# Kernel optimization log

Measured on AMD Instinct MI355X. Metric: run time of the kernel, lower is better.

Reference implementation:

```python
import jax, jax.numpy as jnp
import numpy as np

EMBED_DIM = 128
N_HEADS = 8
TANH_CLIP = 10.0
NEG_INF = -1e9


def setup_inputs() -> dict:
    key = jax.random.key(0)
    k1, k2, k3, k4 = jax.random.split(key, 4)
    B, N, D = 512, 200, EMBED_DIM
    s = 1.0 / np.sqrt(D)
    return {
        "embeddings": jax.random.normal(k1, (B, N, D), dtype=jnp.float32),
        "W_node": jax.random.uniform(k2, (D, 3 * D), jnp.float32, -s, s),
        "W_fixed": jax.random.uniform(k3, (D, D), jnp.float32, -s, s),
        "W_step": jax.random.uniform(k4, (D, D), jnp.float32, -s, s),
    }


def _decode(embeddings, W_node, W_fixed, W_step):
    B, N, D = embeddings.shape
    H = N_HEADS
    dk = D // H

    # Precompute (once): glimpse K/V and logit K, plus fixed graph context.
    proj = embeddings @ W_node                      # [B,N,3D]
    gK, gV, lK = jnp.split(proj, 3, axis=-1)
    gK = gK.reshape(B, N, H, dk).transpose(0, 2, 1, 3)   # [B,H,N,dk]
    gV = gV.reshape(B, N, H, dk).transpose(0, 2, 1, 3)   # [B,H,N,dk]
    graph_emb = embeddings.mean(axis=1)             # [B,D]
    fixed_ctx = graph_emb @ W_fixed                 # [B,D]

    inv_sqrt_dk = 1.0 / jnp.sqrt(jnp.asarray(dk, embeddings.dtype))
    inv_sqrt_d = 1.0 / jnp.sqrt(jnp.asarray(D, embeddings.dtype))
    batch_idx = jnp.arange(B)

    def step(carry, _):
        visited, ctx_emb = carry                    # [B,N] bool, [B,D]
        q = fixed_ctx + ctx_emb @ W_step            # [B,D]
        qh = q.reshape(B, H, dk)                    # [B,H,dk]
        # glimpse multi-head attention (mask_inner=True)
        compat = jnp.einsum('bhd,bhnd->bhn', qh, gK) * inv_sqrt_dk
        compat = jnp.where(visited[:, None, :], NEG_INF, compat)
        attn = jax.nn.softmax(compat, axis=-1)
        glimpse = jnp.einsum('bhn,bhnd->bhd', attn, gV).reshape(B, D)
        # single-head logits with tanh clipping (mask_logits=True)
        logits = jnp.einsum('bd,bnd->bn', glimpse, lK) * inv_sqrt_d
        logits = TANH_CLIP * jnp.tanh(logits)
        logits = jnp.where(visited, NEG_INF, logits)
        log_p = jax.nn.log_softmax(logits, axis=-1)  # [B,N]
        sel = jnp.argmax(log_p, axis=-1)             # greedy [B]
        visited = visited.at[batch_idx, sel].set(True)
        ctx_emb = embeddings[batch_idx, sel]         # next step context
        return (visited, ctx_emb), (log_p, sel)

    init = (jnp.zeros((B, N), dtype=bool), graph_emb)
    _, (log_ps, sels) = jax.lax.scan(step, init, None, length=N)
    return log_ps.transpose(1, 0, 2), sels.transpose(1, 0)  # [B,T,N], [B,T]


def reference(embeddings, W_node, W_fixed, W_step):
    log_p, pi = _decode(embeddings, W_node, W_fixed, W_step)
    return log_p, pi
```

## Files before the change

### kernel.cpp

```cpp
#include <hip/hip_runtime.h>
#include <math.h>


#define Bsz 512
#define Nn  200
#define Dd  128
#define TANH_CLIP 10.0f
#define NEG_INF  -1e9f
#define LOG2E 1.4426950408889634f
#define LN2   0.6931471805599453f

__device__ __forceinline__ float dot4(float4 a, float4 b) {
    return a.x*b.x + a.y*b.y + a.z*b.z + a.w*b.w;
}
__device__ __forceinline__ float rdlane(float v, int l) {
    union { float f; int i; } u; u.f = v;
    u.i = __builtin_amdgcn_readlane(u.i, l);
    return u.f;
}

__global__ __launch_bounds__(256, 3) void proj_kernel(
    const float* __restrict__ emb, const float* __restrict__ Wn,
    float* __restrict__ gk, float* __restrict__ gv, float* __restrict__ lk)
{
    const int bid = blockIdx.x;
    const int cg  = bid % 3;
    const int rowBase = (bid / 3) * 64;
    const int t  = threadIdx.x;
    const int c4 = t & 31;
    const int r8 = t >> 5;

    __shared__ __align__(16) float wn_s[64][128];
    __shared__ __align__(16) float e_s[64][68];

    float acc[8][4];
#pragma unroll
    for (int j = 0; j < 8; ++j)
#pragma unroll
        for (int m = 0; m < 4; ++m) acc[j][m] = 0.f;

    for (int kh = 0; kh < 2; ++kh) {
#pragma unroll
        for (int i = 0; i < 8; ++i) {
            const int idx = t + 256 * i;
            const int kr = idx >> 5, cc = (idx & 31) * 4;
            *(float4*)&wn_s[kr][cc] =
                *(const float4*)&Wn[(size_t)(kh * 64 + kr) * 384 + 128 * cg + cc];
        }
#pragma unroll
        for (int i = 0; i < 4; ++i) {
            const int idx = t + 256 * i;
            const int rr = idx >> 4, kk4 = (idx & 15) * 4;
            *(float4*)&e_s[rr][kk4] =
                *(const float4*)&emb[(size_t)(rowBase + rr) * Dd + kh * 64 + kk4];
        }
        __syncthreads();

#pragma unroll
        for (int k4 = 0; k4 < 16; ++k4) {
            float4 er[8];
#pragma unroll
            for (int j = 0; j < 8; ++j)
                er[j] = *(const float4*)&e_s[8 * r8 + j][4 * k4];
#pragma unroll
            for (int m = 0; m < 4; ++m) {
                const float4 wv = *(const float4*)&wn_s[4 * k4 + m][4 * c4];
#pragma unroll
                for (int j = 0; j < 8; ++j) {
                    const float ev = (m == 0) ? er[j].x : (m == 1) ? er[j].y
                                   : (m == 2) ? er[j].z : er[j].w;
                    acc[j][0] = fmaf(ev, wv.x, acc[j][0]);
                    acc[j][1] = fmaf(ev, wv.y, acc[j][1]);
                    acc[j][2] = fmaf(ev, wv.z, acc[j][2]);
                    acc[j][3] = fmaf(ev, wv.w, acc[j][3]);
                }
            }
        }
        __syncthreads();
    }

    float* out = (cg == 0) ? gk : (cg == 1) ? gv : lk;
#pragma unroll
    for (int j = 0; j < 8; ++j) {
        float4 v; v.x = acc[j][0]; v.y = acc[j][1]; v.z = acc[j][2]; v.w = acc[j][3];
        *(float4*)&out[(size_t)(rowBase + 8 * r8 + j) * Dd + 4 * c4] = v;
    }
}

__global__ __launch_bounds__(512, 1) void decode_kernel(
    const float* __restrict__ emb,
    const float* __restrict__ Wf,
    const float* __restrict__ Wsp,
    const float* __restrict__ gk, const float* __restrict__ gv,
    const float* __restrict__ lk,
    float* __restrict__ out_logp,
    float* __restrict__ out_pi)
{
    const int b    = blockIdx.x;
    const int t    = threadIdx.x;
    const int lane = t & 63;
    const int w    = t >> 6;
    const int g    = t >> 7;
    const int d    = t & 127;
    const int jq   = lane >> 2;
    const int cq   = lane & 3;

    __shared__ __align__(16) float qall_s[201 * Dd];
    __shared__ __align__(16) float wchunk_s[16][Dd];
    __shared__ __align__(16) float sm2[8][256];
    __shared__ __align__(16) float red[4][Dd];
    __shared__ __align__(16) float ctx0_s[Dd];
    __shared__ __align__(16) float fixedc_s[Dd];
    __shared__ __align__(16) float glim_s[Dd];
    __shared__ __align__(16) float logits_s[Nn];

    const float inv_sqrt_d = 0.08838834764831845f;
    const float QSCALE = 0.25f * LOG2E;

    const float* embB = emb + (size_t)b * Nn * Dd;
    const float* gkB  = gk  + (size_t)b * Nn * Dd;
    const float* gvB  = gv  + (size_t)b * Nn * Dd;
    const float* lkB  = lk  + (size_t)b * Nn * Dd;

    {
        const float4* e4  = (const float4*)embB;
        float4*       es4 = (float4*)qall_s;
#pragma unroll
        for (int it = 0; it < 12; ++it) es4[t + 512 * it] = e4[t + 512 * it];
        if (t < 256) es4[t + 6144] = e4[t + 6144];
    }
    __syncthreads();

    {
        float s = 0.f;
#pragma unroll
        for (int k = 0; k < 50; ++k) s += qall_s[(50 * g + k) * Dd + d];
        red[g][d] = s;
    }
    __syncthreads();
    if (t < 128) ctx0_s[t] = (red[0][t] + red[1][t] + red[2][t] + red[3][t]) * (1.0f / 200.0f);
    __syncthreads();

    {
        float s = 0.f;
#pragma unroll
        for (int j = 0; j < 32; ++j)
            s = fmaf(ctx0_s[32 * g + j], Wf[(32 * g + j) * Dd + d], s);
        red[g][d] = s;
    }
    __syncthreads();
    if (t < 128) {
        fixedc_s[t] = (red[0][t] + red[1][t] + red[2][t] + red[3][t]) * QSCALE;
        qall_s[200 * Dd + t] = ctx0_s[t];
    }
    __syncthreads();

    float qr[52];
#pragma unroll
    for (int i = 0; i < 52; ++i) qr[i] = 0.f;

    for (int kc = 0; kc < 8; ++kc) {
        {
            const int kr = t >> 5, cc = (t & 31) * 4;
            *(float4*)&wchunk_s[kr][cc] =
                *(const float4*)&Wsp[(size_t)(16 * kc + kr) * Dd + cc];
        }
        __syncthreads();
#pragma unroll
        for (int i = 0; i < 52; ++i) {
            const int r = 52 * g + i;
            if (r < 201) {
#pragma unroll
                for (int j4 = 0; j4 < 4; ++j4) {
                    const float4 ev = *(const float4*)&qall_s[r * Dd + 16 * kc + 4 * j4];
                    qr[i] = fmaf(ev.x, wchunk_s[4 * j4 + 0][d], qr[i]);
                    qr[i] = fmaf(ev.y, wchunk_s[4 * j4 + 1][d], qr[i]);
                    qr[i] = fmaf(ev.z, wchunk_s[4 * j4 + 2][d], qr[i]);
                    qr[i] = fmaf(ev.w, wchunk_s[4 * j4 + 3][d], qr[i]);
                }
            }
        }
        __syncthreads();
    }
#pragma unroll
    for (int i = 0; i < 52; ++i) {
        const int r = 52 * g + i;
        if (r < 201) qall_s[r * Dd + d] = qr[i] * QSCALE;
    }
    __syncthreads();

    float4 gk0[4], gk1[4], gk2[4], gk3[4];
    float  gv_r[52];
    float4 lk_r[16];
    {
        const float4* s0 = (const float4*)(gkB + (size_t)(lane      ) * Dd + 16 * w);
        const float4* s1 = (const float4*)(gkB + (size_t)(lane +  64) * Dd + 16 * w);
        const float4* s2 = (const float4*)(gkB + (size_t)(lane + 128) * Dd + 16 * w);
        const int n3 = (lane < 8) ? lane + 192 : 199;
        const float4* s3 = (const float4*)(gkB + (size_t)n3 * Dd + 16 * w);
#pragma unroll
        for (int i = 0; i < 4; ++i) { gk0[i]=s0[i]; gk1[i]=s1[i]; gk2[i]=s2[i]; gk3[i]=s3[i]; }
    }
#pragma unroll
    for (int k = 0; k < 52; ++k) {
        int r = 52 * cq + k; r = r < 200 ? r : 199;
        gv_r[k] = gvB[(size_t)r * Dd + 16 * w + jq];
    }
    if (t < 400) {
        const float4* src = (const float4*)(lkB + (size_t)(t >> 1) * Dd + (t & 1) * 64);
#pragma unroll
        for (int i = 0; i < 16; ++i) lk_r[i] = src[i];
    } else {
#pragma unroll
        for (int i = 0; i < 16; ++i) lk_r[i] = float4{0, 0, 0, 0};
    }
    const float fc_q = fixedc_s[16 * w + jq];

    unsigned long long vis0 = 0, vis1 = 0, vis2 = 0, vis3 = 0;
    int sel_prev = 200;

    for (int step = 0; step < Nn; ++step) {
        float s = qall_s[sel_prev * Dd + 16 * w + jq] + fc_q;
        const float q0  = rdlane(s, 0),  q1  = rdlane(s, 4),  q2  = rdlane(s, 8),  q3  = rdlane(s, 12);
        const float q4  = rdlane(s, 16), q5  = rdlane(s, 20), q6  = rdlane(s, 24), q7  = rdlane(s, 28);
        const float q8  = rdlane(s, 32), q9  = rdlane(s, 36), q10 = rdlane(s, 40), q11 = rdlane(s, 44);
        const float q12 = rdlane(s, 48), q13 = rdlane(s, 52), q14 = rdlane(s, 56), q15 = rdlane(s, 60);

#define DOT16(G) (fmaf((G)[0].x,q0, fmaf((G)[0].y,q1, fmaf((G)[0].z,q2, fmaf((G)[0].w,q3, \
                  fmaf((G)[1].x,q4, fmaf((G)[1].y,q5, fmaf((G)[1].z,q6, fmaf((G)[1].w,q7, \
                  fmaf((G)[2].x,q8, fmaf((G)[2].y,q9, fmaf((G)[2].z,q10,fmaf((G)[2].w,q11,\
                  fmaf((G)[3].x,q12,fmaf((G)[3].y,q13,fmaf((G)[3].z,q14,(G)[3].w*q15))))))))))))))))

        float x0 = DOT16(gk0), x1 = DOT16(gk1), x2 = DOT16(gk2), x3 = DOT16(gk3);
        x0 = ((vis0 >> lane) & 1ull) ? -1e30f : x0;
        x1 = ((vis1 >> lane) & 1ull) ? -1e30f : x1;
        x2 = ((vis2 >> lane) & 1ull) ? -1e30f : x2;
        x3 = (lane < 8 && !((vis3 >> lane) & 1ull)) ? x3 : -1e30f;
        const float p0 = exp2f(x0), p1 = exp2f(x1), p2 = exp2f(x2), p3 = exp2f(x3);
        {
            float* prow = &sm2[w][0];
            prow[lane      ] = p0;
            prow[lane +  64] = p1;
            prow[lane + 128] = p2;
            prow[lane + 192] = p3;
        }
        float ps = (p0 + p1) + (p2 + p3);
#pragma unroll
        for (int off = 1; off < 64; off <<= 1) ps += __shfl_xor(ps, off);
        const float invps = 1.0f / ps;

        {
            const float* a = &sm2[w][52 * cq];
            float s0 = 0.f, s1 = 0.f, s2 = 0.f, s3 = 0.f;
#pragma unroll
            for (int k4 = 0; k4 < 13; ++k4) {
                const float4 av = ((const float4*)a)[k4];
                s0 = fmaf(av.x, gv_r[4 * k4 + 0], s0);
                s1 = fmaf(av.y, gv_r[4 * k4 + 1], s1);
                s2 = fmaf(av.z, gv_r[4 * k4 + 2], s2);
                s3 = fmaf(av.w, gv_r[4 * k4 + 3], s3);
            }
            float gsum = (s0 + s1) + (s2 + s3);
            gsum += __shfl_xor(gsum, 1);
            gsum += __shfl_xor(gsum, 2);
            if (cq == 0) glim_s[16 * w + jq] = gsum * invps;
        }
        __syncthreads();

        if (t < 400) {
            const int n = t >> 1, jh = t & 1;
            const float4* gl = ((const float4*)glim_s) + 16 * jh;
            float a0 = 0.f, a1 = 0.f, a2 = 0.f, a3 = 0.f;
#pragma unroll
            for (int i = 0; i < 4; ++i) {
                const float4 l0 = lk_r[4*i+0], l1 = lk_r[4*i+1], l2 = lk_r[4*i+2], l3 = lk_r[4*i+3];
                const float4 g0 = gl[4*i+0],  g1 = gl[4*i+1],  g2 = gl[4*i+2],  g3 = gl[4*i+3];
                a0 = fmaf(l0.x,g0.x, fmaf(l0.y,g0.y, fmaf(l0.z,g0.z, fmaf(l0.w,g0.w, a0))));
                a1 = fmaf(l1.x,g1.x, fmaf(l1.y,g1.y, fmaf(l1.z,g1.z, fmaf(l1.w,g1.w, a1))));
                a2 = fmaf(l2.x,g2.x, fmaf(l2.y,g2.y, fmaf(l2.z,g2.z, fmaf(l2.w,g2.w, a2))));
                a3 = fmaf(l3.x,g3.x, fmaf(l3.y,g3.y, fmaf(l3.z,g3.z, fmaf(l3.w,g3.w, a3))));
            }
            float sl = (a0 + a1) + (a2 + a3);
            sl += __shfl_xor(sl, 1);
            if (jh == 0) {
                const float xx = sl * inv_sqrt_d;
                const float u  = exp2f(xx * (2.0f * LOG2E));
                const float th = 1.0f - 2.0f / (u + 1.0f);
                const int w2 = n >> 6, bit = n & 63;
                const unsigned long long mw = (w2 == 0) ? vis0 : (w2 == 1) ? vis1
                                            : (w2 == 2) ? vis2 : vis3;
                logits_s[n] = ((mw >> bit) & 1ull) ? NEG_INF : TANH_CLIP * th;
            }
        }
        __syncthreads();

        const float v0 = logits_s[lane], v1 = logits_s[lane + 64], v2 = logits_s[lane + 128];
        const float v3 = (lane < 8) ? logits_s[lane + 192] : -INFINITY;
        float mx = fmaxf(fmaxf(v0, v1), fmaxf(v2, v3));
        float e0 = exp2f((v0 - 10.f) * LOG2E) + exp2f((v1 - 10.f) * LOG2E)
                 + exp2f((v2 - 10.f) * LOG2E)
                 + ((lane < 8) ? exp2f((v3 - 10.f) * LOG2E) : 0.f);
#pragma unroll
        for (int off = 1; off < 64; off <<= 1) {
            mx = fmaxf(mx, __shfl_xor(mx, off));
            e0 += __shfl_xor(e0, off);
        }
        const unsigned long long b0 = __ballot(v0 == mx);
        const unsigned long long b1 = __ballot(v1 == mx);
        const unsigned long long b2 = __ballot(v2 == mx);
        const unsigned long long b3 = __ballot(v3 == mx);
        const int sel = b0 ? __builtin_ctzll(b0)
                      : b1 ? 64  + __builtin_ctzll(b1)
                      : b2 ? 128 + __builtin_ctzll(b2)
                      :      192 + __builtin_ctzll(b3);
        const float lse = log2f(e0) * LN2 + 10.f;

        if (t < 50) {
            float4 lv = *(const float4*)&logits_s[4 * t];
            lv.x -= lse; lv.y -= lse; lv.z -= lse; lv.w -= lse;
            *(float4*)&out_logp[((size_t)b * Nn + step) * Nn + 4 * t] = lv;
        }
        if (t == 0) out_pi[(size_t)b * Nn + step] = (float)sel;
        const unsigned long long sbit = 1ull << (sel & 63);
        const int sw = sel >> 6;
        vis0 |= (sw == 0) ? sbit : 0ull;
        vis1 |= (sw == 1) ? sbit : 0ull;
        vis2 |= (sw == 2) ? sbit : 0ull;
        vis3 |= (sw == 3) ? sbit : 0ull;
        sel_prev = sel;
    }
#undef DOT16
}

extern "C" void kernel_launch(void* const* d_in, const int* in_sizes, int n_in,
                              void* d_out, int out_size, void* d_ws, size_t ws_size,
                              hipStream_t stream) {
    (void)in_sizes; (void)n_in; (void)out_size; (void)ws_size;
    const float* emb = (const float*)d_in[0];
    const float* Wn  = (const float*)d_in[1];
    const float* Wf  = (const float*)d_in[2];
    const float* Wsp = (const float*)d_in[3];

    const size_t BND = (size_t)Bsz * Nn * Dd;
    float* gk = (float*)d_ws;
    float* gv = gk + BND;
    float* lk = gv + BND;

    float* out_logp = (float*)d_out;
    float* out_pi   = out_logp + (size_t)Bsz * Nn * Nn;

    proj_kernel<<<(Bsz * Nn / 64) * 3, 256, 0, stream>>>(emb, Wn, gk, gv, lk);
    decode_kernel<<<Bsz, 512, 0, stream>>>(emb, Wf, Wsp, gk, gv, lk,
                                           out_logp, out_pi);
}
```

Baseline: 1.154 ms.

## Compute step query on the fly, fold scales into projection, use packed FMA

Removes the big per-block precompute of all 201 query rows (qall_s, about 100KB of LDS). Each step now computes q from the selected embedding row using W_step columns held in registers, and the fixed-context term is folded into a per-key bias. The fixed-context/mean prep moves to a separate small kernel. The Q and logit scales are folded into the projection outputs, dot products use packed v2f FMA and a fast reciprocal, and launch bounds allow more resident blocks. The trade-off is an extra global row load and reduction on the serial per-step path, higher register pressure, and slightly different rounding.

```diff
diff --git a/kernel.cpp b/kernel.cpp
--- a/kernel.cpp
+++ b/kernel.cpp
@@ -9,14 +9,35 @@
 #define NEG_INF  -1e9f
 #define LOG2E 1.4426950408889634f
 #define LN2   0.6931471805599453f
-
-__device__ __forceinline__ float dot4(float4 a, float4 b) {
-    return a.x*b.x + a.y*b.y + a.z*b.z + a.w*b.w;
+#define QSCALE (0.25f * LOG2E)
+#define LSCALE (0.08838834764831845f * 2.0f * LOG2E)
+
+typedef float v2f __attribute__((ext_vector_type(2)));
+
+__device__ __forceinline__ v2f pkfma(v2f a, v2f b, v2f c) {
+    return __builtin_elementwise_fma(a, b, c);
 }
 __device__ __forceinline__ float rdlane(float v, int l) {
     union { float f; int i; } u; u.f = v;
     u.i = __builtin_amdgcn_readlane(u.i, l);
     return u.f;
+}
+__device__ __forceinline__ float fast_rcp(float x) {
+    return __builtin_amdgcn_rcpf(x);
+}
+__device__ __forceinline__ float dot16pk(const float4* g4, const float4* q4) {
+    const v2f* g = (const v2f*)g4;
+    const v2f* q = (const v2f*)q4;
+    v2f a0 = g[0] * q[0];
+    v2f a1 = g[1] * q[1];
+    a0 = pkfma(g[2], q[2], a0);
+    a1 = pkfma(g[3], q[3], a1);
+    a0 = pkfma(g[4], q[4], a0);
+    a1 = pkfma(g[5], q[5], a1);
+    a0 = pkfma(g[6], q[6], a0);
+    a1 = pkfma(g[7], q[7], a1);
+    const v2f a = a0 + a1;
+    return a.x + a.y;
 }
 
 __global__ __launch_bounds__(256, 3) void proj_kernel(
@@ -80,19 +101,42 @@
     }
 
     float* out = (cg == 0) ? gk : (cg == 1) ? gv : lk;
+    const float scl = (cg == 0) ? QSCALE : (cg == 2) ? LSCALE : 1.0f;
 #pragma unroll
     for (int j = 0; j < 8; ++j) {
-        float4 v; v.x = acc[j][0]; v.y = acc[j][1]; v.z = acc[j][2]; v.w = acc[j][3];
+        float4 v;
+        v.x = acc[j][0] * scl; v.y = acc[j][1] * scl;
+        v.z = acc[j][2] * scl; v.w = acc[j][3] * scl;
         *(float4*)&out[(size_t)(rowBase + 8 * r8 + j) * Dd + 4 * c4] = v;
     }
 }
 
-__global__ __launch_bounds__(512, 1) void decode_kernel(
+__global__ __launch_bounds__(128) void ctxprep_kernel(
+    const float* __restrict__ emb, const float* __restrict__ Wf,
+    float* __restrict__ fixedc, float* __restrict__ ctx0row)
+{
+    const int b = blockIdx.x, d = threadIdx.x;
+    __shared__ float c0[Dd];
+    const float* e = emb + (size_t)b * Nn * Dd;
+    float s = 0.f;
+#pragma unroll 4
+    for (int n = 0; n < Nn; ++n) s += e[n * Dd + d];
+    s *= (1.0f / (float)Nn);
+    c0[d] = s;
+    ctx0row[(size_t)b * Dd + d] = s;
+    __syncthreads();
+    float f = 0.f;
+#pragma unroll 8
+    for (int k = 0; k < Dd; ++k) f = fmaf(c0[k], Wf[k * Dd + d], f);
+    fixedc[(size_t)b * Dd + d] = f;
+}
+
+__global__ __launch_bounds__(512, 4) void decode_kernel(
     const float* __restrict__ emb,
-    const float* __restrict__ Wf,
     const float* __restrict__ Wsp,
     const float* __restrict__ gk, const float* __restrict__ gv,
     const float* __restrict__ lk,
+    const float* __restrict__ fixedc, const float* __restrict__ ctx0row,
     float* __restrict__ out_logp,
     float* __restrict__ out_pi)
 {
@@ -100,98 +144,24 @@
     const int t    = threadIdx.x;
     const int lane = t & 63;
     const int w    = t >> 6;
-    const int g    = t >> 7;
-    const int d    = t & 127;
     const int jq   = lane >> 2;
-    const int cq   = lane & 3;
-
-    __shared__ __align__(16) float qall_s[201 * Dd];
-    __shared__ __align__(16) float wchunk_s[16][Dd];
+    const int kk   = lane & 3;
+
     __shared__ __align__(16) float sm2[8][256];
-    __shared__ __align__(16) float red[4][Dd];
-    __shared__ __align__(16) float ctx0_s[Dd];
-    __shared__ __align__(16) float fixedc_s[Dd];
     __shared__ __align__(16) float glim_s[Dd];
     __shared__ __align__(16) float logits_s[Nn];
-
-    const float inv_sqrt_d = 0.08838834764831845f;
-    const float QSCALE = 0.25f * LOG2E;
 
     const float* embB = emb + (size_t)b * Nn * Dd;
     const float* gkB  = gk  + (size_t)b * Nn * Dd;
     const float* gvB  = gv  + (size_t)b * Nn * Dd;
     const float* lkB  = lk  + (size_t)b * Nn * Dd;
 
-    {
-        const float4* e4  = (const float4*)embB;
-        float4*       es4 = (float4*)qall_s;
-#pragma unroll
-        for (int it = 0; it < 12; ++it) es4[t + 512 * it] = e4[t + 512 * it];
-        if (t < 256) es4[t + 6144] = e4[t + 6144];
-    }
-    __syncthreads();
-
-    {
-        float s = 0.f;
-#pragma unroll
-        for (int k = 0; k < 50; ++k) s += qall_s[(50 * g + k) * Dd + d];
-        red[g][d] = s;
-    }
-    __syncthreads();
-    if (t < 128) ctx0_s[t] = (red[0][t] + red[1][t] + red[2][t] + red[3][t]) * (1.0f / 200.0f);
-    __syncthreads();
-
-    {
-        float s = 0.f;
-#pragma unroll
-        for (int j = 0; j < 32; ++j)
-            s = fmaf(ctx0_s[32 * g + j], Wf[(32 * g + j) * Dd + d], s);
-        red[g][d] = s;
-    }
-    __syncthreads();
-    if (t < 128) {
-        fixedc_s[t] = (red[0][t] + red[1][t] + red[2][t] + red[3][t]) * QSCALE;
-        qall_s[200 * Dd + t] = ctx0_s[t];
-    }
-    __syncthreads();
-
-    float qr[52];
-#pragma unroll
-    for (int i = 0; i < 52; ++i) qr[i] = 0.f;
-
-    for (int kc = 0; kc < 8; ++kc) {
-        {
-            const int kr = t >> 5, cc = (t & 31) * 4;
-            *(float4*)&wchunk_s[kr][cc] =
-                *(const float4*)&Wsp[(size_t)(16 * kc + kr) * Dd + cc];
-        }
-        __syncthreads();
-#pragma unroll
-        for (int i = 0; i < 52; ++i) {
-            const int r = 52 * g + i;
-            if (r < 201) {
-#pragma unroll
-                for (int j4 = 0; j4 < 4; ++j4) {
-                    const float4 ev = *(const float4*)&qall_s[r * Dd + 16 * kc + 4 * j4];
-                    qr[i] = fmaf(ev.x, wchunk_s[4 * j4 + 0][d], qr[i]);
-                    qr[i] = fmaf(ev.y, wchunk_s[4 * j4 + 1][d], qr[i]);
-                    qr[i] = fmaf(ev.z, wchunk_s[4 * j4 + 2][d], qr[i]);
-                    qr[i] = fmaf(ev.w, wchunk_s[4 * j4 + 3][d], qr[i]);
-                }
-            }
-        }
-        __syncthreads();
-    }
-#pragma unroll
-    for (int i = 0; i < 52; ++i) {
-        const int r = 52 * g + i;
-        if (r < 201) qall_s[r * Dd + d] = qr[i] * QSCALE;
-    }
-    __syncthreads();
-
     float4 gk0[4], gk1[4], gk2[4], gk3[4];
-    float  gv_r[52];
-    float4 lk_r[16];
+    float  wsa[32];
+    float  gva[52];
+    float  lka[64];
+    float  cb0, cb1, cb2, cb3;
+
     {
         const float4* s0 = (const float4*)(gkB + (size_t)(lane      ) * Dd + 16 * w);
         const float4* s1 = (const float4*)(gkB + (size_t)(lane +  64) * Dd + 16 * w);
@@ -202,94 +172,121 @@
         for (int i = 0; i < 4; ++i) { gk0[i]=s0[i]; gk1[i]=s1[i]; gk2[i]=s2[i]; gk3[i]=s3[i]; }
     }
 #pragma unroll
+    for (int j = 0; j < 32; ++j)
+        wsa[j] = Wsp[(size_t)(32 * kk + j) * Dd + 16 * w + jq];
+#pragma unroll
     for (int k = 0; k < 52; ++k) {
-        int r = 52 * cq + k; r = r < 200 ? r : 199;
-        gv_r[k] = gvB[(size_t)r * Dd + 16 * w + jq];
+        int r = 52 * kk + k; r = r < 200 ? r : 199;
+        gva[k] = gvB[(size_t)r * Dd + 16 * w + jq];
     }
     if (t < 400) {
         const float4* src = (const float4*)(lkB + (size_t)(t >> 1) * Dd + (t & 1) * 64);
 #pragma unroll
-        for (int i = 0; i < 16; ++i) lk_r[i] = src[i];
+        for (int i = 0; i < 16; ++i) *(float4*)&lka[4 * i] = src[i];
     } else {
 #pragma unroll
-        for (int i = 0; i < 16; ++i) lk_r[i] = float4{0, 0, 0, 0};
-    }
-    const float fc_q = fixedc_s[16 * w + jq];
+        for (int i = 0; i < 64; ++i) lka[i] = 0.f;
+    }
+    {
+        float4 fcf[4];
+        const float4* fcp = (const float4*)(fixedc + (size_t)b * Dd + 16 * w);
+#pragma unroll
+        for (int i = 0; i < 4; ++i) fcf[i] = fcp[i];
+        cb0 = dot16pk(gk0, fcf);
+        cb1 = dot16pk(gk1, fcf);
+        cb2 = dot16pk(gk2, fcf);
+        cb3 = dot16pk(gk3, fcf);
+    }
 
     unsigned long long vis0 = 0, vis1 = 0, vis2 = 0, vis3 = 0;
-    int sel_prev = 200;
+    int sel_prev = -1;
 
     for (int step = 0; step < Nn; ++step) {
-        float s = qall_s[sel_prev * Dd + 16 * w + jq] + fc_q;
-        const float q0  = rdlane(s, 0),  q1  = rdlane(s, 4),  q2  = rdlane(s, 8),  q3  = rdlane(s, 12);
-        const float q4  = rdlane(s, 16), q5  = rdlane(s, 20), q6  = rdlane(s, 24), q7  = rdlane(s, 28);
-        const float q8  = rdlane(s, 32), q9  = rdlane(s, 36), q10 = rdlane(s, 40), q11 = rdlane(s, 44);
-        const float q12 = rdlane(s, 48), q13 = rdlane(s, 52), q14 = rdlane(s, 56), q15 = rdlane(s, 60);
-
-#define DOT16(G) (fmaf((G)[0].x,q0, fmaf((G)[0].y,q1, fmaf((G)[0].z,q2, fmaf((G)[0].w,q3, \
-                  fmaf((G)[1].x,q4, fmaf((G)[1].y,q5, fmaf((G)[1].z,q6, fmaf((G)[1].w,q7, \
-                  fmaf((G)[2].x,q8, fmaf((G)[2].y,q9, fmaf((G)[2].z,q10,fmaf((G)[2].w,q11,\
-                  fmaf((G)[3].x,q12,fmaf((G)[3].y,q13,fmaf((G)[3].z,q14,(G)[3].w*q15))))))))))))))))
-
-        float x0 = DOT16(gk0), x1 = DOT16(gk1), x2 = DOT16(gk2), x3 = DOT16(gk3);
-        x0 = ((vis0 >> lane) & 1ull) ? -1e30f : x0;
-        x1 = ((vis1 >> lane) & 1ull) ? -1e30f : x1;
-        x2 = ((vis2 >> lane) & 1ull) ? -1e30f : x2;
-        x3 = (lane < 8 && !((vis3 >> lane) & 1ull)) ? x3 : -1e30f;
-        const float p0 = exp2f(x0), p1 = exp2f(x1), p2 = exp2f(x2), p3 = exp2f(x3);
+        const float* rowp = (step == 0) ? (ctx0row + (size_t)b * Dd)
+                                        : (embB + (size_t)sel_prev * Dd);
         {
+            const float4* c4 = (const float4*)(rowp + 32 * kk);
+            const v2f* wsv = (const v2f*)wsa;
+            v2f a0 = {0.f, 0.f}, a1 = {0.f, 0.f};
+#pragma unroll
+            for (int i = 0; i < 8; i += 2) {
+                const float4 ca = c4[i], cb = c4[i + 1];
+                a0 = pkfma((v2f){ca.x, ca.y}, wsv[2 * i + 0], a0);
+                a1 = pkfma((v2f){ca.z, ca.w}, wsv[2 * i + 1], a1);
+                a0 = pkfma((v2f){cb.x, cb.y}, wsv[2 * i + 2], a0);
+                a1 = pkfma((v2f){cb.z, cb.w}, wsv[2 * i + 3], a1);
+            }
+            const v2f a = a0 + a1;
+            float s = a.x + a.y;
+            s += __shfl_xor(s, 1);
+            s += __shfl_xor(s, 2);
+            float4 qf[4];
+            qf[0].x = rdlane(s, 0);  qf[0].y = rdlane(s, 4);
+            qf[0].z = rdlane(s, 8);  qf[0].w = rdlane(s, 12);
+            qf[1].x = rdlane(s, 16); qf[1].y = rdlane(s, 20);
+            qf[1].z = rdlane(s, 24); qf[1].w = rdlane(s, 28);
+            qf[2].x = rdlane(s, 32); qf[2].y = rdlane(s, 36);
+            qf[2].z = rdlane(s, 40); qf[2].w = rdlane(s, 44);
+            qf[3].x = rdlane(s, 48); qf[3].y = rdlane(s, 52);
+            qf[3].z = rdlane(s, 56); qf[3].w = rdlane(s, 60);
+
+            float x0 = dot16pk(gk0, qf) + cb0;
+            float x1 = dot16pk(gk1, qf) + cb1;
+            float x2 = dot16pk(gk2, qf) + cb2;
+            float x3 = dot16pk(gk3, qf) + cb3;
+            x0 = ((vis0 >> lane) & 1ull) ? -1e30f : x0;
+            x1 = ((vis1 >> lane) & 1ull) ? -1e30f : x1;
+            x2 = ((vis2 >> lane) & 1ull) ? -1e30f : x2;
+            x3 = (lane < 8 && !((vis3 >> lane) & 1ull)) ? x3 : -1e30f;
+            const float p0 = exp2f(x0), p1 = exp2f(x1), p2 = exp2f(x2), p3 = exp2f(x3);
             float* prow = &sm2[w][0];
             prow[lane      ] = p0;
             prow[lane +  64] = p1;
             prow[lane + 128] = p2;
             prow[lane + 192] = p3;
-        }
-        float ps = (p0 + p1) + (p2 + p3);
-#pragma unroll
-        for (int off = 1; off < 64; off <<= 1) ps += __shfl_xor(ps, off);
-        const float invps = 1.0f / ps;
-
-        {
-            const float* a = &sm2[w][52 * cq];
-            float s0 = 0.f, s1 = 0.f, s2 = 0.f, s3 = 0.f;
-#pragma unroll
-            for (int k4 = 0; k4 < 13; ++k4) {
-                const float4 av = ((const float4*)a)[k4];
-                s0 = fmaf(av.x, gv_r[4 * k4 + 0], s0);
-                s1 = fmaf(av.y, gv_r[4 * k4 + 1], s1);
-                s2 = fmaf(av.z, gv_r[4 * k4 + 2], s2);
-                s3 = fmaf(av.w, gv_r[4 * k4 + 3], s3);
-            }
-            float gsum = (s0 + s1) + (s2 + s3);
+            float ps = (p0 + p1) + (p2 + p3);
+#pragma unroll
+            for (int off = 1; off < 64; off <<= 1) ps += __shfl_xor(ps, off);
+            const float invps = fast_rcp(ps);
+
+            const v2f* av = (const v2f*)(&sm2[w][52 * kk]);
+            const v2f* gvv = (const v2f*)gva;
+            v2f g0 = {0.f, 0.f}, g1 = {0.f, 0.f};
+#pragma unroll
+            for (int k2 = 0; k2 < 26; k2 += 2) {
+                g0 = pkfma(av[k2], gvv[k2], g0);
+                g1 = pkfma(av[k2 + 1], gvv[k2 + 1], g1);
+            }
+            const v2f gt = g0 + g1;
+            float gsum = gt.x + gt.y;
             gsum += __shfl_xor(gsum, 1);
             gsum += __shfl_xor(gsum, 2);
-            if (cq == 0) glim_s[16 * w + jq] = gsum * invps;
+            if (kk == 0) glim_s[16 * w + jq] = gsum * invps;
         }
         __syncthreads();
 
         if (t < 400) {
             const int n = t >> 1, jh = t & 1;
-            const float4* gl = ((const float4*)glim_s) + 16 * jh;
-            float a0 = 0.f, a1 = 0.f, a2 = 0.f, a3 = 0.f;
-#pragma unroll
-            for (int i = 0; i < 4; ++i) {
-                const float4 l0 = lk_r[4*i+0], l1 = lk_r[4*i+1], l2 = lk_r[4*i+2], l3 = lk_r[4*i+3];
-                const float4 g0 = gl[4*i+0],  g1 = gl[4*i+1],  g2 = gl[4*i+2],  g3 = gl[4*i+3];
-                a0 = fmaf(l0.x,g0.x, fmaf(l0.y,g0.y, fmaf(l0.z,g0.z, fmaf(l0.w,g0.w, a0))));
-                a1 = fmaf(l1.x,g1.x, fmaf(l1.y,g1.y, fmaf(l1.z,g1.z, fmaf(l1.w,g1.w, a1))));
-                a2 = fmaf(l2.x,g2.x, fmaf(l2.y,g2.y, fmaf(l2.z,g2.z, fmaf(l2.w,g2.w, a2))));
-                a3 = fmaf(l3.x,g3.x, fmaf(l3.y,g3.y, fmaf(l3.z,g3.z, fmaf(l3.w,g3.w, a3))));
-            }
-            float sl = (a0 + a1) + (a2 + a3);
+            const v2f* gl = (const v2f*)(glim_s + 64 * jh);
+            const v2f* lv = (const v2f*)lka;
+            v2f a0 = {0.f,0.f}, a1 = {0.f,0.f}, a2 = {0.f,0.f}, a3 = {0.f,0.f};
+#pragma unroll
+            for (int i = 0; i < 32; i += 4) {
+                a0 = pkfma(lv[i + 0], gl[i + 0], a0);
+                a1 = pkfma(lv[i + 1], gl[i + 1], a1);
+                a2 = pkfma(lv[i + 2], gl[i + 2], a2);
+                a3 = pkfma(lv[i + 3], gl[i + 3], a3);
+            }
+            const v2f at = (a0 + a1) + (a2 + a3);
+            float sl = at.x + at.y;
             sl += __shfl_xor(sl, 1);
             if (jh == 0) {
-                const float xx = sl * inv_sqrt_d;
-                const float u  = exp2f(xx * (2.0f * LOG2E));
-                const float th = 1.0f - 2.0f / (u + 1.0f);
+                const float u = exp2f(sl);
+                const float v = TANH_CLIP - 2.0f * TANH_CLIP * fast_rcp(u + 1.0f);
                 const int w2 = n >> 6, bit = n & 63;
                 const unsigned long long mw = (w2 == 0) ? vis0 : (w2 == 1) ? vis1
                                             : (w2 == 2) ? vis2 : vis3;
-                logits_s[n] = ((mw >> bit) & 1ull) ? NEG_INF : TANH_CLIP * th;
+                logits_s[n] = ((mw >> bit) & 1ull) ? NEG_INF : v;
             }
         }
         __syncthreads();
@@ -316,9 +313,9 @@
         const float lse = log2f(e0) * LN2 + 10.f;
 
         if (t < 50) {
-            float4 lv = *(const float4*)&logits_s[4 * t];
-            lv.x -= lse; lv.y -= lse; lv.z -= lse; lv.w -= lse;
-            *(float4*)&out_logp[((size_t)b * Nn + step) * Nn + 4 * t] = lv;
+            float4 lv4 = *(const float4*)&logits_s[4 * t];
+            lv4.x -= lse; lv4.y -= lse; lv4.z -= lse; lv4.w -= lse;
+            *(float4*)&out_logp[((size_t)b * Nn + step) * Nn + 4 * t] = lv4;
         }
         if (t == 0) out_pi[(size_t)b * Nn + step] = (float)sel;
         const unsigned long long sbit = 1ull << (sel & 63);
@@ -329,7 +326,6 @@
         vis3 |= (sw == 3) ? sbit : 0ull;
         sel_prev = sel;
     }
-#undef DOT16
 }
 
 extern "C" void kernel_launch(void* const* d_in, const int* in_sizes, int n_in,
@@ -342,14 +338,17 @@
     const float* Wsp = (const float*)d_in[3];
 
     const size_t BND = (size_t)Bsz * Nn * Dd;
-    float* gk = (float*)d_ws;
-    float* gv = gk + BND;
-    float* lk = gv + BND;
+    float* gk      = (float*)d_ws;
+    float* gv      = gk + BND;
+    float* lk      = gv + BND;
+    float* fixedc  = lk + BND;
+    float* ctx0row = fixedc + (size_t)Bsz * Dd;
 
     float* out_logp = (float*)d_out;
     float* out_pi   = out_logp + (size_t)Bsz * Nn * Nn;
 
     proj_kernel<<<(Bsz * Nn / 64) * 3, 256, 0, stream>>>(emb, Wn, gk, gv, lk);
-    decode_kernel<<<Bsz, 512, 0, stream>>>(emb, Wf, Wsp, gk, gv, lk,
+    ctxprep_kernel<<<Bsz, 128, 0, stream>>>(emb, Wf, fixedc, ctx0row);
+    decode_kernel<<<Bsz, 512, 0, stream>>>(emb, Wsp, gk, gv, lk, fixedc, ctx0row,
                                            out_logp, out_pi);
 }
```

Result: slower. 4.567 ms (+295.8%).

## Redistribute logit dot across waves, fold scales into projection, cut per-step barriers

Applied to the files above, without the earlier changes.

The logit-key tensor is now loaded with the same per-wave 16-dimension layout as the glimpse keys. Each wave computes its glimpse slice and partial logit dots locally, and the partials are reduced through a double-buffered shared array, so one block-wide barrier per step replaces the earlier glimpse and logit barriers. The QSCALE and tanh scale factors move into the projection kernel's output, and the fixed-context term of the compatibility is precomputed once per node. Packed two-wide FMAs and a fast reciprocal replace scalar code. This adds some shared-memory traffic for the partial sums and slightly changes rounding.

```diff
diff --git a/kernel.cpp b/kernel.cpp
--- a/kernel.cpp
+++ b/kernel.cpp
@@ -9,14 +9,30 @@
 #define NEG_INF  -1e9f
 #define LOG2E 1.4426950408889634f
 #define LN2   0.6931471805599453f
-
-__device__ __forceinline__ float dot4(float4 a, float4 b) {
-    return a.x*b.x + a.y*b.y + a.z*b.z + a.w*b.w;
-}
-__device__ __forceinline__ float rdlane(float v, int l) {
-    union { float f; int i; } u; u.f = v;
-    u.i = __builtin_amdgcn_readlane(u.i, l);
-    return u.f;
+#define QSCALE (0.25f * LOG2E)
+#define LSCALE (0.08838834764831845f * 2.0f * LOG2E)
+
+typedef float v2f __attribute__((ext_vector_type(2)));
+
+__device__ __forceinline__ v2f pkfma(v2f a, v2f b, v2f c) {
+    return __builtin_elementwise_fma(a, b, c);
+}
+__device__ __forceinline__ float fast_rcp(float x) {
+    return __builtin_amdgcn_rcpf(x);
+}
+__device__ __forceinline__ float dot16pk(const float4* g4, const float4* q4) {
+    const v2f* g = (const v2f*)g4;
+    const v2f* q = (const v2f*)q4;
+    v2f a0 = g[0] * q[0];
+    v2f a1 = g[1] * q[1];
+    a0 = pkfma(g[2], q[2], a0);
+    a1 = pkfma(g[3], q[3], a1);
+    a0 = pkfma(g[4], q[4], a0);
+    a1 = pkfma(g[5], q[5], a1);
+    a0 = pkfma(g[6], q[6], a0);
+    a1 = pkfma(g[7], q[7], a1);
+    const v2f a = a0 + a1;
+    return a.x + a.y;
 }
 
 __global__ __launch_bounds__(256, 3) void proj_kernel(
@@ -80,14 +96,17 @@
     }
 
     float* out = (cg == 0) ? gk : (cg == 1) ? gv : lk;
+    const float scl = (cg == 0) ? QSCALE : (cg == 2) ? LSCALE : 1.0f;
 #pragma unroll
     for (int j = 0; j < 8; ++j) {
-        float4 v; v.x = acc[j][0]; v.y = acc[j][1]; v.z = acc[j][2]; v.w = acc[j][3];
+        float4 v;
+        v.x = acc[j][0] * scl; v.y = acc[j][1] * scl;
+        v.z = acc[j][2] * scl; v.w = acc[j][3] * scl;
         *(float4*)&out[(size_t)(rowBase + 8 * r8 + j) * Dd + 4 * c4] = v;
     }
 }
 
-__global__ __launch_bounds__(512, 1) void decode_kernel(
+__global__ __launch_bounds__(512, 2) void decode_kernel(
     const float* __restrict__ emb,
     const float* __restrict__ Wf,
     const float* __restrict__ Wsp,
@@ -103,19 +122,16 @@
     const int g    = t >> 7;
     const int d    = t & 127;
     const int jq   = lane >> 2;
-    const int cq   = lane & 3;
+    const int kk   = lane & 3;
 
     __shared__ __align__(16) float qall_s[201 * Dd];
     __shared__ __align__(16) float wchunk_s[16][Dd];
     __shared__ __align__(16) float sm2[8][256];
+    __shared__ __align__(16) float glimbc[8][16];
+    __shared__             float smp[2][256][9];
     __shared__ __align__(16) float red[4][Dd];
     __shared__ __align__(16) float ctx0_s[Dd];
     __shared__ __align__(16) float fixedc_s[Dd];
-    __shared__ __align__(16) float glim_s[Dd];
-    __shared__ __align__(16) float logits_s[Nn];
-
-    const float inv_sqrt_d = 0.08838834764831845f;
-    const float QSCALE = 0.25f * LOG2E;
 
     const float* embB = emb + (size_t)b * Nn * Dd;
     const float* gkB  = gk  + (size_t)b * Nn * Dd;
@@ -150,7 +166,7 @@
     }
     __syncthreads();
     if (t < 128) {
-        fixedc_s[t] = (red[0][t] + red[1][t] + red[2][t] + red[3][t]) * QSCALE;
+        fixedc_s[t] = red[0][t] + red[1][t] + red[2][t] + red[3][t];
         qall_s[200 * Dd + t] = ctx0_s[t];
     }
     __syncthreads();
@@ -185,13 +201,14 @@
 #pragma unroll
     for (int i = 0; i < 52; ++i) {
         const int r = 52 * g + i;
-        if (r < 201) qall_s[r * Dd + d] = qr[i] * QSCALE;
+        if (r < 201) qall_s[r * Dd + d] = qr[i];
     }
     __syncthreads();
 
     float4 gk0[4], gk1[4], gk2[4], gk3[4];
-    float  gv_r[52];
-    float4 lk_r[16];
+    float4 lk0[4], lk1[4], lk2[4], lk3[4];
+    float  gva[52];
+    float  cb0, cb1, cb2, cb3;
     {
         const float4* s0 = (const float4*)(gkB + (size_t)(lane      ) * Dd + 16 * w);
         const float4* s1 = (const float4*)(gkB + (size_t)(lane +  64) * Dd + 16 * w);
@@ -200,38 +217,44 @@
         const float4* s3 = (const float4*)(gkB + (size_t)n3 * Dd + 16 * w);
 #pragma unroll
         for (int i = 0; i < 4; ++i) { gk0[i]=s0[i]; gk1[i]=s1[i]; gk2[i]=s2[i]; gk3[i]=s3[i]; }
+        const float4* l0 = (const float4*)(lkB + (size_t)(lane      ) * Dd + 16 * w);
+        const float4* l1 = (const float4*)(lkB + (size_t)(lane +  64) * Dd + 16 * w);
+        const float4* l2 = (const float4*)(lkB + (size_t)(lane + 128) * Dd + 16 * w);
+        const float4* l3 = (const float4*)(lkB + (size_t)n3 * Dd + 16 * w);
+#pragma unroll
+        for (int i = 0; i < 4; ++i) { lk0[i]=l0[i]; lk1[i]=l1[i]; lk2[i]=l2[i]; lk3[i]=l3[i]; }
     }
 #pragma unroll
     for (int k = 0; k < 52; ++k) {
-        int r = 52 * cq + k; r = r < 200 ? r : 199;
-        gv_r[k] = gvB[(size_t)r * Dd + 16 * w + jq];
-    }
-    if (t < 400) {
-        const float4* src = (const float4*)(lkB + (size_t)(t >> 1) * Dd + (t & 1) * 64);
-#pragma unroll
-        for (int i = 0; i < 16; ++i) lk_r[i] = src[i];
-    } else {
-#pragma unroll
-        for (int i = 0; i < 16; ++i) lk_r[i] = float4{0, 0, 0, 0};
-    }
-    const float fc_q = fixedc_s[16 * w + jq];
+        int r = 52 * kk + k; r = r < 200 ? r : 199;
+        gva[k] = gvB[(size_t)r * Dd + 16 * w + jq];
+    }
+    {
+        float4 fcf[4];
+        const float4* fcp = (const float4*)(fixedc_s + 16 * w);
+#pragma unroll
+        for (int i = 0; i < 4; ++i) fcf[i] = fcp[i];
+        cb0 = dot16pk(gk0, fcf);
+        cb1 = dot16pk(gk1, fcf);
+        cb2 = dot16pk(gk2, fcf);
+        cb3 = dot16pk(gk3, fcf);
+    }
 
     unsigned long long vis0 = 0, vis1 = 0, vis2 = 0, vis3 = 0;
     int sel_prev = 200;
+    int par = 0;
 
     for (int step = 0; step < Nn; ++step) {
-        float s = qall_s[sel_prev * Dd + 16 * w + jq] + fc_q;
-        const float q0  = rdlane(s, 0),  q1  = rdlane(s, 4),  q2  = rdlane(s, 8),  q3  = rdlane(s, 12);
-        const float q4  = rdlane(s, 16), q5  = rdlane(s, 20), q6  = rdlane(s, 24), q7  = rdlane(s, 28);
-        const float q8  = rdlane(s, 32), q9  = rdlane(s, 36), q10 = rdlane(s, 40), q11 = rdlane(s, 44);
-        const float q12 = rdlane(s, 48), q13 = rdlane(s, 52), q14 = rdlane(s, 56), q15 = rdlane(s, 60);
-
-#define DOT16(G) (fmaf((G)[0].x,q0, fmaf((G)[0].y,q1, fmaf((G)[0].z,q2, fmaf((G)[0].w,q3, \
-                  fmaf((G)[1].x,q4, fmaf((G)[1].y,q5, fmaf((G)[1].z,q6, fmaf((G)[1].w,q7, \
-                  fmaf((G)[2].x,q8, fmaf((G)[2].y,q9, fmaf((G)[2].z,q10,fmaf((G)[2].w,q11,\
-                  fmaf((G)[3].x,q12,fmaf((G)[3].y,q13,fmaf((G)[3].z,q14,(G)[3].w*q15))))))))))))))))
-
-        float x0 = DOT16(gk0), x1 = DOT16(gk1), x2 = DOT16(gk2), x3 = DOT16(gk3);
+        float4 qf[4];
+        {
+            const float4* qp = (const float4*)(qall_s + sel_prev * Dd + 16 * w);
+            qf[0] = qp[0]; qf[1] = qp[1]; qf[2] = qp[2]; qf[3] = qp[3];
+        }
+
+        float x0 = dot16pk(gk0, qf) + cb0;
+        float x1 = dot16pk(gk1, qf) + cb1;
+        float x2 = dot16pk(gk2, qf) + cb2;
+        float x3 = dot16pk(gk3, qf) + cb3;
         x0 = ((vis0 >> lane) & 1ull) ? -1e30f : x0;
         x1 = ((vis1 >> lane) & 1ull) ? -1e30f : x1;
         x2 = ((vis2 >> lane) & 1ull) ? -1e30f : x2;
@@ -247,80 +270,79 @@
         float ps = (p0 + p1) + (p2 + p3);
 #pragma unroll
         for (int off = 1; off < 64; off <<= 1) ps += __shfl_xor(ps, off);
-        const float invps = 1.0f / ps;
-
-        {
-            const float* a = &sm2[w][52 * cq];
-            float s0 = 0.f, s1 = 0.f, s2 = 0.f, s3 = 0.f;
-#pragma unroll
-            for (int k4 = 0; k4 < 13; ++k4) {
-                const float4 av = ((const float4*)a)[k4];
-                s0 = fmaf(av.x, gv_r[4 * k4 + 0], s0);
-                s1 = fmaf(av.y, gv_r[4 * k4 + 1], s1);
-                s2 = fmaf(av.z, gv_r[4 * k4 + 2], s2);
-                s3 = fmaf(av.w, gv_r[4 * k4 + 3], s3);
+        const float invps = fast_rcp(ps);
+
+        {
+            const v2f* av  = (const v2f*)(&sm2[w][52 * kk]);
+            const v2f* gvv = (const v2f*)gva;
+            v2f g0 = {0.f, 0.f}, g1 = {0.f, 0.f};
+#pragma unroll
+            for (int k2 = 0; k2 < 26; k2 += 2) {
+                g0 = pkfma(av[k2],     gvv[k2],     g0);
+                g1 = pkfma(av[k2 + 1], gvv[k2 + 1], g1);
             }
-            float gsum = (s0 + s1) + (s2 + s3);
+            const v2f gt = g0 + g1;
+            float gsum = gt.x + gt.y;
             gsum += __shfl_xor(gsum, 1);
             gsum += __shfl_xor(gsum, 2);
-            if (cq == 0) glim_s[16 * w + jq] = gsum * invps;
-        }
-        __syncthreads();
-
-        if (t < 400) {
-            const int n = t >> 1, jh = t & 1;
-            const float4* gl = ((const float4*)glim_s) + 16 * jh;
-            float a0 = 0.f, a1 = 0.f, a2 = 0.f, a3 = 0.f;
-#pragma unroll
-            for (int i = 0; i < 4; ++i) {
-                const float4 l0 = lk_r[4*i+0], l1 = lk_r[4*i+1], l2 = lk_r[4*i+2], l3 = lk_r[4*i+3];
-                const float4 g0 = gl[4*i+0],  g1 = gl[4*i+1],  g2 = gl[4*i+2],  g3 = gl[4*i+3];
-                a0 = fmaf(l0.x,g0.x, fmaf(l0.y,g0.y, fmaf(l0.z,g0.z, fmaf(l0.w,g0.w, a0))));
-                a1 = fmaf(l1.x,g1.x, fmaf(l1.y,g1.y, fmaf(l1.z,g1.z, fmaf(l1.w,g1.w, a1))));
-                a2 = fmaf(l2.x,g2.x, fmaf(l2.y,g2.y, fmaf(l2.z,g2.z, fmaf(l2.w,g2.w, a2))));
-                a3 = fmaf(l3.x,g3.x, fmaf(l3.y,g3.y, fmaf(l3.z,g3.z, fmaf(l3.w,g3.w, a3))));
-            }
-            float sl = (a0 + a1) + (a2 + a3);
-            sl += __shfl_xor(sl, 1);
-            if (jh == 0) {
-                const float xx = sl * inv_sqrt_d;
-                const float u  = exp2f(xx * (2.0f * LOG2E));
-                const float th = 1.0f - 2.0f / (u + 1.0f);
-                const int w2 = n >> 6, bit = n & 63;
-                const unsigned long long mw = (w2 == 0) ? vis0 : (w2 == 1) ? vis1
-                                            : (w2 == 2) ? vis2 : vis3;
-                logits_s[n] = ((mw >> bit) & 1ull) ? NEG_INF : TANH_CLIP * th;
-            }
-        }
-        __syncthreads();
-
-        const float v0 = logits_s[lane], v1 = logits_s[lane + 64], v2 = logits_s[lane + 128];
-        const float v3 = (lane < 8) ? logits_s[lane + 192] : -INFINITY;
-        float mx = fmaxf(fmaxf(v0, v1), fmaxf(v2, v3));
-        float e0 = exp2f((v0 - 10.f) * LOG2E) + exp2f((v1 - 10.f) * LOG2E)
-                 + exp2f((v2 - 10.f) * LOG2E)
-                 + ((lane < 8) ? exp2f((v3 - 10.f) * LOG2E) : 0.f);
+            if (kk == 0) glimbc[w][jq] = gsum * invps;
+        }
+        float4 gw[4];
+        {
+            const float4* gbp = (const float4*)&glimbc[w][0];
+            gw[0] = gbp[0]; gw[1] = gbp[1]; gw[2] = gbp[2]; gw[3] = gbp[3];
+        }
+
+        smp[par][lane      ][w] = dot16pk(lk0, gw);
+        smp[par][lane +  64][w] = dot16pk(lk1, gw);
+        smp[par][lane + 128][w] = dot16pk(lk2, gw);
+        smp[par][lane + 192][w] = dot16pk(lk3, gw);
+        __syncthreads();
+
+        float sl0 = 0.f, sl1 = 0.f, sl2 = 0.f, sl3 = 0.f;
+#pragma unroll
+        for (int w2 = 0; w2 < 8; ++w2) {
+            sl0 += smp[par][lane      ][w2];
+            sl1 += smp[par][lane +  64][w2];
+            sl2 += smp[par][lane + 128][w2];
+            sl3 += smp[par][lane + 192][w2];
+        }
+        const float u0 = exp2f(sl0), u1 = exp2f(sl1), u2 = exp2f(sl2), u3 = exp2f(sl3);
+        float l0 = TANH_CLIP - 2.0f * TANH_CLIP * fast_rcp(u0 + 1.0f);
+        float l1 = TANH_CLIP - 2.0f * TANH_CLIP * fast_rcp(u1 + 1.0f);
+        float l2 = TANH_CLIP - 2.0f * TANH_CLIP * fast_rcp(u2 + 1.0f);
+        float l3 = TANH_CLIP - 2.0f * TANH_CLIP * fast_rcp(u3 + 1.0f);
+        l0 = ((vis0 >> lane) & 1ull) ? NEG_INF : l0;
+        l1 = ((vis1 >> lane) & 1ull) ? NEG_INF : l1;
+        l2 = ((vis2 >> lane) & 1ull) ? NEG_INF : l2;
+        l3 = (lane < 8 && !((vis3 >> lane) & 1ull)) ? l3 : NEG_INF;
+
+        float mx = fmaxf(fmaxf(l0, l1), fmaxf(l2, l3));
+        float e0 = exp2f((l0 - 10.f) * LOG2E) + exp2f((l1 - 10.f) * LOG2E)
+                 + exp2f((l2 - 10.f) * LOG2E) + exp2f((l3 - 10.f) * LOG2E);
 #pragma unroll
         for (int off = 1; off < 64; off <<= 1) {
             mx = fmaxf(mx, __shfl_xor(mx, off));
             e0 += __shfl_xor(e0, off);
         }
-        const unsigned long long b0 = __ballot(v0 == mx);
-        const unsigned long long b1 = __ballot(v1 == mx);
-        const unsigned long long b2 = __ballot(v2 == mx);
-        const unsigned long long b3 = __ballot(v3 == mx);
+        const unsigned long long b0 = __ballot(l0 == mx);
+        const unsigned long long b1 = __ballot(l1 == mx);
+        const unsigned long long b2 = __ballot(l2 == mx);
+        const unsigned long long b3 = __ballot(l3 == mx);
         const int sel = b0 ? __builtin_ctzll(b0)
                       : b1 ? 64  + __builtin_ctzll(b1)
                       : b2 ? 128 + __builtin_ctzll(b2)
                       :      192 + __builtin_ctzll(b3);
         const float lse = log2f(e0) * LN2 + 10.f;
 
-        if (t < 50) {
-            float4 lv = *(const float4*)&logits_s[4 * t];
-            lv.x -= lse; lv.y -= lse; lv.z -= lse; lv.w -= lse;
-            *(float4*)&out_logp[((size_t)b * Nn + step) * Nn + 4 * t] = lv;
-        }
-        if (t == 0) out_pi[(size_t)b * Nn + step] = (float)sel;
+        if (w == 0) {
+            float* orow = out_logp + ((size_t)b * Nn + step) * Nn;
+            orow[lane      ] = l0 - lse;
+            orow[lane +  64] = l1 - lse;
+            orow[lane + 128] = l2 - lse;
+            if (lane < 8) orow[lane + 192] = l3 - lse;
+            if (lane == 0) out_pi[(size_t)b * Nn + step] = (float)sel;
+        }
         const unsigned long long sbit = 1ull << (sel & 63);
         const int sw = sel >> 6;
         vis0 |= (sw == 0) ? sbit : 0ull;
@@ -328,8 +350,8 @@
         vis2 |= (sw == 2) ? sbit : 0ull;
         vis3 |= (sw == 3) ? sbit : 0ull;
         sel_prev = sel;
-    }
-#undef DOT16
+        par ^= 1;
+    }
 }
 
 extern "C" void kernel_launch(void* const* d_in, const int* in_sizes, int n_in,
```

Measured after the change: 1.005 ms. -12.9%, faster.
